# Kernel tuning notes

Hardware: AMD Instinct MI355X
Metric: run time of the kernel (lower is better)

## Reference

```python
import jax, jax.numpy as jnp
import numpy as np

T, B, D, H, N = 2048, 8, 1024, 16, 32


def setup_inputs() -> dict:
    key = jax.random.key(0)
    ks = jax.random.split(key, 6)
    s = 1.0 / np.sqrt(D)  # xavier-ish scale
    return {
        "x": jax.random.normal(ks[0], (T, B, D), jnp.float32),
        "S0": jnp.zeros((B, H, N, N), jnp.float32),
        "W_in": jax.random.normal(ks[1], (D, D), jnp.float32) * s,
        "W_k": jax.random.normal(ks[2], (H * N, D), jnp.float32) * s,
        "W_v": jax.random.normal(ks[3], (H * N, D), jnp.float32) * s,
        "W_q": jax.random.normal(ks[4], (H * N, D), jnp.float32) * s,
        "W_beta": jax.random.normal(ks[5], (H * N, D), jnp.float32) * s,
        "b_beta": jnp.full((H, N), 2.0, jnp.float32),  # init_beta_bias=2.0
    }


def reference(x, S0, W_in, W_k, W_v, W_q, W_beta, b_beta):
    # x: [T,B,D] -> in_proj (expansion=1.0 so d_inner == D)
    Tn, Bn, Dn = x.shape
    Hh, Nn = b_beta.shape
    xp = jnp.einsum('tbd,ed->tbe', x, W_in)  # [T,B,D]
    # projections to [T,B,H,N]
    k = jnp.einsum('tbd,fd->tbf', xp, W_k).reshape(Tn, Bn, Hh, Nn)
    v = jnp.einsum('tbd,fd->tbf', xp, W_v).reshape(Tn, Bn, Hh, Nn)
    q = jnp.einsum('tbd,fd->tbf', xp, W_q).reshape(Tn, Bn, Hh, Nn)
    beta = jax.nn.sigmoid(
        jnp.einsum('tbd,fd->tbf', xp, W_beta).reshape(Tn, Bn, Hh, Nn) + b_beta)

    def step(S, inputs):
        # S: [B,H,N,N]; each input: [B,H,N]
        k_t, v_t, q_t, beta_t = inputs
        k_norm = k_t / (jnp.linalg.norm(k_t, axis=-1, keepdims=True) + 1e-6)
        retrieved = jnp.einsum('bhij,bhj->bhi', S, k_norm)
        delta = v_t - retrieved
        outer = delta[..., :, None] * k_norm[..., None, :]  # [B,H,N,N]
        S_new = jnp.tanh(beta_t[..., None] * S + outer)
        Sq = jnp.einsum('bhij,bhj->bhi', S_new, q_t)
        out_t = Sq * (Sq * jax.nn.sigmoid(Sq))  # Sq * silu(Sq)
        return S_new, out_t

    S_final, outs = jax.lax.scan(step, S0, (k, v, q, beta))
    output = outs.reshape(Tn, Bn, Hh * Nn)  # [T,B,H*N]
    return output, S_final
```

## Files before the change

kernel.cpp:

```cpp
#include <hip/hip_runtime.h>
#include <hip/hip_bf16.h>
#include <stdint.h>

#define TT 2048
#define BB 8
#define DD 1024
#define FF 2048
#define HN 512
#define KB_CNT 32
#define ROWB 128
#define MSTRIDE 4096
#define BROWB 64
#define BSTRIDE 2048
#define PF 8

typedef float f32x4 __attribute__((ext_vector_type(4)));
typedef float f32x2 __attribute__((ext_vector_type(2)));
typedef _Float16 h8_t __attribute__((ext_vector_type(8)));

#define CC   2.88539008f
#define SQC  1.69864360f

__device__ __forceinline__ float fexp2(float x){ return __builtin_amdgcn_exp2f(x); }
__device__ __forceinline__ float frcp(float x){ return __builtin_amdgcn_rcpf(x); }
__device__ __forceinline__ float fsqrt_(float x){ return __builtin_amdgcn_sqrtf(x); }
__device__ __forceinline__ float fast_sigmoid(float x){
    return frcp(1.0f + fexp2(-1.44269504f * x));
}

template<int CTRL>
__device__ __forceinline__ float dppadd(float v){
    int x = __builtin_amdgcn_update_dpp(0, __float_as_int(v), CTRL, 0xf, 0xf, true);
    return v + __int_as_float(x);
}
__device__ __forceinline__ float reduce16(float v){
    v = dppadd<0xB1>(v);
    v = dppadd<0x4E>(v);
    v = dppadd<0x141>(v);
    v = dppadd<0x140>(v);
    return v;
}

__device__ __forceinline__ void split8(const float* f, int4& hi, int4& lo){
    union { _Float16 h[8]; int4 i; } a, c;
    #pragma unroll
    for (int u = 0; u < 8; ++u) {
        _Float16 h = (_Float16)f[u];
        a.h[u] = h;
        c.h[u] = (_Float16)(f[u] - (float)h);
    }
    hi = a.i; lo = c.i;
}
__device__ __forceinline__ int4 cvt8(const float* f){
    union { _Float16 h[8]; int4 i; } a;
    #pragma unroll
    for (int u = 0; u < 8; ++u) a.h[u] = (_Float16)f[u];
    return a.i;
}

__global__ __launch_bounds__(256)
void gemm_f32c(const float* __restrict__ s0, const float* __restrict__ s1,
               const float* __restrict__ s2, const float* __restrict__ s3,
               const float* __restrict__ B, float* __restrict__ C)
{
    __shared__ __align__(16) float As[16][68];
    __shared__ __align__(16) float Bs[16][72];
    const int tid = threadIdx.x;
    const int tx = tid & 15, ty = tid >> 4;
    const int n0 = blockIdx.x * 64, m0 = blockIdx.y * 64;
    float acc[4][4] = {};

    const int arow = tid >> 2, ac4 = (tid & 3) << 2;
    const int f = m0 + arow;
    const float* asrc = ((f < 512) ? s0 : (f < 1024) ? s1 : (f < 1536) ? s2 : s3)
                        + (size_t)(f & 511) * DD + ac4;
    const int bk = tid >> 4, bc = tid & 15;

    for (int k0 = 0; k0 < DD; k0 += 16) {
        float4 av = *(const float4*)(asrc + k0);
        As[ac4+0][arow] = av.x; As[ac4+1][arow] = av.y;
        As[ac4+2][arow] = av.z; As[ac4+3][arow] = av.w;
        float4 bv = *(const float4*)&B[(size_t)(k0 + bk) * DD + n0 + bc * 4];
        int p = bc + (bc >> 3);
        *(float4*)&Bs[bk][p << 2] = bv;
        __syncthreads();
        #pragma unroll
        for (int kk = 0; kk < 16; ++kk) {
            float a[4], b[4];
            *(float4*)&a[0] = *(const float4*)&As[kk][ty * 4];
            int p2 = tx + (tx >> 3);
            *(float4*)&b[0] = *(const float4*)&Bs[kk][p2 << 2];
            #pragma unroll
            for (int i = 0; i < 4; ++i)
                #pragma unroll
                for (int j = 0; j < 4; ++j)
                    acc[i][j] = __builtin_fmaf(a[i], b[j], acc[i][j]);
        }
        __syncthreads();
    }
    #pragma unroll
    for (int ii = 0; ii < 4; ++ii) {
        float4 v;
        v.x = acc[ii][0]; v.y = acc[ii][1]; v.z = acc[ii][2]; v.w = acc[ii][3];
        *(float4*)&C[(size_t)(m0 + ty * 4 + ii) * DD + n0 + tx * 4] = v;
    }
}

__global__ __launch_bounds__(256)
void wconv(const float* __restrict__ W, char* __restrict__ out)
{
    int gid = blockIdx.x * 256 + threadIdx.x;
    int n  = gid >> 6;
    int kh = gid & 63;
    const float* src = W + (size_t)n * DD + kh * 16;
    float f[16];
    *(float4*)&f[0]  = *(const float4*)(src + 0);
    *(float4*)&f[4]  = *(const float4*)(src + 4);
    *(float4*)&f[8]  = *(const float4*)(src + 8);
    *(float4*)&f[12] = *(const float4*)(src + 12);
    int4 hi0, hi1, lo0, lo1;
    split8(&f[0], hi0, lo0);
    split8(&f[8], hi1, lo1);
    int kb = kh >> 1, c0 = (kh & 1) * 2, rs = n & 7;
    char* dst = out + (size_t)n * MSTRIDE + kb * ROWB;
    *(int4*)(dst + (((c0+0) ^ rs) * 16)) = hi0;
    *(int4*)(dst + (((c0+1) ^ rs) * 16)) = hi1;
    *(int4*)(dst + (((c0+4) ^ rs) * 16)) = lo0;
    *(int4*)(dst + (((c0+5) ^ rs) * 16)) = lo1;
}

__global__ __launch_bounds__(256)
void wconv2(const float* __restrict__ W, char* __restrict__ out)
{
    int gid = blockIdx.x * 256 + threadIdx.x;
    int n  = gid >> 6;
    int kh = gid & 63;
    const float* src = W + (size_t)n * DD + kh * 16;
    float f[16];
    *(float4*)&f[0]  = *(const float4*)(src + 0);
    *(float4*)&f[4]  = *(const float4*)(src + 4);
    *(float4*)&f[8]  = *(const float4*)(src + 8);
    *(float4*)&f[12] = *(const float4*)(src + 12);
    int4 h0 = cvt8(&f[0]);
    int4 h1 = cvt8(&f[8]);
    int kb = kh >> 1, c0 = (kh & 1) * 2, rs = n & 3;
    char* dst = out + (size_t)n * BSTRIDE + kb * BROWB;
    *(int4*)(dst + (((c0+0) ^ rs) * 16)) = h0;
    *(int4*)(dst + (((c0+1) ^ rs) * 16)) = h1;
}

#define EPI_STORE(Cb, rbase, reg, hh, idx, blk, v, bb) { \
    char* rowp = (char*)(Cb) + (size_t)((rbase) + (reg)) * 8192 + (hh) * 512; \
    int sub_ = ((blk) == 0) ? 0 : ((blk) == 2) ? 1 : ((blk) == 1) ? 2 : 3; \
    float v_ = (v); \
    if ((blk) == 1) v_ = SQC * v_; \
    else if ((blk) == 3) v_ = CC * fast_sigmoid(v_ + (bb)); \
    *(float*)(rowp + sub_ * 128 + (idx) * 4) = v_; \
}

__global__ __launch_bounds__(512, 1)
void gemm_mfma8(const char* __restrict__ Axp, const char* __restrict__ Wsp,
                float* __restrict__ C, const float* __restrict__ bias)
{
    extern __shared__ char ldsb[];
    const int tid  = threadIdx.x;
    const int wave = tid >> 6, lane = tid & 63;
    const int wm = wave >> 2, wn = wave & 3;
    const int nt = blockIdx.x & 7, mt = blockIdx.x >> 3;
    const int m0 = mt * 256, n0 = nt * 256;

    f32x4 acc[8][4] = {};

    const char* aT = Axp + (size_t)(m0 + wave * 32 + (lane >> 3)) * MSTRIDE + (lane & 7) * 16;
    const char* bT = Wsp + (size_t)(n0 + wave * 32 + (lane >> 2)) * BSTRIDE + (lane & 3) * 16;
    const int ldstA = wave * 32 * 128;
    const int ldstB = wave * 32 * 64;

    const int fl = lane & 15, fh = lane >> 4;
    const int shiA = (fh ^ (fl & 7)) * 16;
    const int sloA = ((fh + 4) ^ (fl & 7)) * 16;
    const int shiB = (fh ^ (fl & 3)) * 16;

    {
        char* L = ldsb;
        #pragma unroll
        for (int g = 0; g < 4; ++g)
            __builtin_amdgcn_global_load_lds(
                (const __attribute__((address_space(1))) uint32_t*)(aT + (size_t)g * 8 * MSTRIDE),
                (__attribute__((address_space(3))) uint32_t*)(L + ldstA + g * 1024),
                16, 0, 0);
        #pragma unroll
        for (int g = 0; g < 2; ++g)
            __builtin_amdgcn_global_load_lds(
                (const __attribute__((address_space(1))) uint32_t*)(bT + (size_t)g * 16 * BSTRIDE),
                (__attribute__((address_space(3))) uint32_t*)(L + 32768 + ldstB + g * 1024),
                16, 0, 0);
    }

    union u8 { int4 i; h8_t h; };
    u8 Ah[4], Al[4], Bf[4];

    for (int t = 0; t < KB_CNT; ++t) {
        char* Lc = ldsb + (t & 1) * 49152;
        char* Ln = ldsb + ((t + 1) & 1) * 49152;
        const bool stg = (t + 1 < KB_CNT);
        const char* aN = aT + ROWB;
        const char* bN = bT + BROWB;

        asm volatile("s_waitcnt vmcnt(0)" ::: "memory");
        __builtin_amdgcn_s_barrier();
        asm volatile("" ::: "memory");

        if (stg) {
            #pragma unroll
            for (int g = 0; g < 4; ++g)
                __builtin_amdgcn_global_load_lds(
                    (const __attribute__((address_space(1))) uint32_t*)(aN + (size_t)g * 8 * MSTRIDE),
                    (__attribute__((address_space(3))) uint32_t*)(Ln + ldstA + g * 1024),
                    16, 0, 0);
            #pragma unroll
            for (int g = 0; g < 2; ++g)
                __builtin_amdgcn_global_load_lds(
                    (const __attribute__((address_space(1))) uint32_t*)(bN + (size_t)g * 16 * BSTRIDE),
                    (__attribute__((address_space(3))) uint32_t*)(Ln + 32768 + ldstB + g * 1024),
                    16, 0, 0);
        }

        #pragma unroll
        for (int f = 0; f < 4; ++f) {
            const char* base = Lc + 32768 + (wn * 64 + f * 16 + fl) * 64;
            Bf[f].i = *(const int4*)(base + shiB);
        }

        #pragma unroll
        for (int f = 0; f < 4; ++f) {
            const char* base = Lc + (wm * 128 + f * 16 + fl) * 128;
            Ah[f].i = *(const int4*)(base + shiA);
            Al[f].i = *(const int4*)(base + sloA);
        }
        __builtin_amdgcn_s_setprio(1);
        #pragma unroll
        for (int i = 0; i < 4; ++i)
            #pragma unroll
            for (int j = 0; j < 4; ++j)
                acc[i][j] = __builtin_amdgcn_mfma_f32_16x16x32_f16(Ah[i].h, Bf[j].h, acc[i][j], 0, 0, 0);
        #pragma unroll
        for (int i = 0; i < 4; ++i)
            #pragma unroll
            for (int j = 0; j < 4; ++j)
                acc[i][j] = __builtin_amdgcn_mfma_f32_16x16x32_f16(Al[i].h, Bf[j].h, acc[i][j], 0, 0, 0);
        __builtin_amdgcn_s_setprio(0);

        #pragma unroll
        for (int f = 0; f < 4; ++f) {
            const char* base = Lc + (wm * 128 + (f + 4) * 16 + fl) * 128;
            Ah[f].i = *(const int4*)(base + shiA);
            Al[f].i = *(const int4*)(base + sloA);
        }
        __builtin_amdgcn_s_setprio(1);
        #pragma unroll
        for (int i = 0; i < 4; ++i)
            #pragma unroll
            for (int j = 0; j < 4; ++j)
                acc[i + 4][j] = __builtin_amdgcn_mfma_f32_16x16x32_f16(Ah[i].h, Bf[j].h, acc[i + 4][j], 0, 0, 0);
        #pragma unroll
        for (int i = 0; i < 4; ++i)
            #pragma unroll
            for (int j = 0; j < 4; ++j)
                acc[i + 4][j] = __builtin_amdgcn_mfma_f32_16x16x32_f16(Al[i].h, Bf[j].h, acc[i + 4][j], 0, 0, 0);
        __builtin_amdgcn_s_setprio(0);

        aT += ROWB; bT += BROWB;
    }

    const int blk = nt >> 1;
    if (blk == 0) {
        #pragma unroll
        for (int fm = 0; fm < 8; ++fm)
            #pragma unroll
            for (int hg = 0; hg < 2; ++hg)
                #pragma unroll
                for (int reg = 0; reg < 4; ++reg) {
                    float a = acc[fm][hg*2][reg], c = acc[fm][hg*2+1][reg];
                    float p = __builtin_fmaf(a, a, c * c);
                    p = reduce16(p);
                    float rn = SQC * frcp(fsqrt_(p) + 1e-6f);
                    acc[fm][hg*2][reg]   = a * rn;
                    acc[fm][hg*2+1][reg] = c * rn;
                }
    }

    #pragma unroll
    for (int fm = 0; fm < 8; ++fm) {
        int rbase = m0 + wm * 128 + fm * 16 + fh * 4;
        #pragma unroll
        for (int fn = 0; fn < 4; ++fn) {
            int col = n0 + wn * 64 + fn * 16 + fl;
            int hh  = (col >> 5) & 15;
            int idx = col & 31;
            float bb = (blk == 3) ? bias[col - 3 * HN] : 0.0f;
            #pragma unroll
            for (int reg = 0; reg < 4; ++reg) {
                float v = acc[fm][fn][reg];
                EPI_STORE(C, rbase, reg, hh, idx, blk, v, bb);
            }
        }
    }
}

__global__ __launch_bounds__(256)
void gemm_mfma(const float* __restrict__ A, const char* __restrict__ Wsp,
               float* __restrict__ C, const float* __restrict__ bias)
{
    __shared__ char lds[24576];
    char* Asb = lds;
    char* Bsb = lds + 16384;

    const int tid  = threadIdx.x;
    const int wave = tid >> 6, lane = tid & 63;
    const int wm = wave >> 1, wn = wave & 1;
    const int nt = blockIdx.x & 15, mt = blockIdx.x >> 4;
    const int m0 = mt * 128, n0 = nt * 128;

    f32x4 acc[4][4] = {};

    const int ar = tid >> 1, akh = tid & 1, ars = ar & 7, ac0 = akh * 2;
    const float* asrc = A + (size_t)(m0 + ar) * DD + akh * 16;
    char* awr = Asb + ar * ROWB;

    const char* bsrc_base = Wsp + (size_t)n0 * BSTRIDE;

    const int fl = lane & 15, fh = lane >> 4;
    const int shiA = (fh ^ (fl & 7)) * 16;
    const int sloA = ((fh + 4) ^ (fl & 7)) * 16;
    const int shiB = (fh ^ (fl & 3)) * 16;

    for (int ks = 0; ks < KB_CNT; ++ks) {
        #pragma unroll
        for (int gg = 0; gg < 2; ++gg) {
            int g = wave * 2 + gg;
            const char* src = bsrc_base + (size_t)(g * 16 + (lane >> 2)) * BSTRIDE
                              + ks * BROWB + (lane & 3) * 16;
            __builtin_amdgcn_global_load_lds(
                (const __attribute__((address_space(1))) uint32_t*)src,
                (__attribute__((address_space(3))) uint32_t*)(Bsb + g * 1024),
                16, 0, 0);
        }
        {
            const float* ap = asrc + ks * 32;
            float f[16];
            *(float4*)&f[0]  = *(const float4*)(ap + 0);
            *(float4*)&f[4]  = *(const float4*)(ap + 4);
            *(float4*)&f[8]  = *(const float4*)(ap + 8);
            *(float4*)&f[12] = *(const float4*)(ap + 12);
            int4 hi0, hi1, lo0, lo1;
            split8(&f[0], hi0, lo0);
            split8(&f[8], hi1, lo1);
            *(int4*)(awr + (((ac0+0) ^ ars) * 16)) = hi0;
            *(int4*)(awr + (((ac0+1) ^ ars) * 16)) = hi1;
            *(int4*)(awr + (((ac0+4) ^ ars) * 16)) = lo0;
            *(int4*)(awr + (((ac0+5) ^ ars) * 16)) = lo1;
        }
        __syncthreads();

        union { int4 i; h8_t h; } ah[4], al[4], bf[4];
        #pragma unroll
        for (int fm = 0; fm < 4; ++fm) {
            const char* base = Asb + (wm * 64 + fm * 16 + fl) * ROWB;
            ah[fm].i = *(const int4*)(base + shiA);
            al[fm].i = *(const int4*)(base + sloA);
        }
        #pragma unroll
        for (int fn = 0; fn < 4; ++fn) {
            const char* base = Bsb + (wn * 64 + fn * 16 + fl) * BROWB;
            bf[fn].i = *(const int4*)(base + shiB);
        }
        #pragma unroll
        for (int fm = 0; fm < 4; ++fm)
            #pragma unroll
            for (int fn = 0; fn < 4; ++fn) {
                acc[fm][fn] = __builtin_amdgcn_mfma_f32_16x16x32_f16(ah[fm].h, bf[fn].h, acc[fm][fn], 0, 0, 0);
                acc[fm][fn] = __builtin_amdgcn_mfma_f32_16x16x32_f16(al[fm].h, bf[fn].h, acc[fm][fn], 0, 0, 0);
            }
        __syncthreads();
    }

    const int blk = nt >> 2;
    if (blk == 0) {
        #pragma unroll
        for (int fm = 0; fm < 4; ++fm)
            #pragma unroll
            for (int hg = 0; hg < 2; ++hg)
                #pragma unroll
                for (int reg = 0; reg < 4; ++reg) {
                    float a = acc[fm][hg*2][reg], c = acc[fm][hg*2+1][reg];
                    float p = __builtin_fmaf(a, a, c * c);
                    p = reduce16(p);
                    float rn = SQC * frcp(fsqrt_(p) + 1e-6f);
                    acc[fm][hg*2][reg]   = a * rn;
                    acc[fm][hg*2+1][reg] = c * rn;
                }
    }

    #pragma unroll
    for (int fm = 0; fm < 4; ++fm) {
        int rbase = m0 + wm * 64 + fm * 16 + fh * 4;
        #pragma unroll
        for (int fn = 0; fn < 4; ++fn) {
            int col = n0 + wn * 64 + fn * 16 + fl;
            int hh  = (col >> 5) & 15;
            int idx = col & 31;
            float bb = (blk == 3) ? bias[col - 3 * HN] : 0.0f;
            #pragma unroll
            for (int reg = 0; reg < 4; ++reg) {
                float v = acc[fm][fn][reg];
                EPI_STORE(C, rbase, reg, hh, idx, blk, v, bb);
            }
        }
    }
}

__global__ __launch_bounds__(256)
void recur(const float* __restrict__ proj, const float* __restrict__ S0,
           float* __restrict__ out, float* __restrict__ Sfin)
{
    const int tid = threadIdx.x;
    const int bx  = blockIdx.x;
    const int bh  = bx >> 1;
    const int b   = bh >> 4, h = bh & 15;
    const int i   = ((bx & 1) << 4) + (tid >> 4);
    const int jl  = tid & 15;

    f32x2 S;
    {
        const float* s0p = S0 + (size_t)bh * 1024 + i * 32 + 2 * jl;
        S[0] = s0p[0]; S[1] = s0p[1];
    }

    const char* pkq = (const char*)proj + (size_t)b * 8192 + h * 512 + jl * 8;
    const char* pvb = (const char*)proj + (size_t)b * 8192 + h * 512 + 256 + i * 4;
    const size_t rstep = (size_t)BB * 8192;

    f32x2 K2[PF], Q2[PF];
    float V[PF], Bt[PF];

    #pragma unroll
    for (int p = 0; p < PF; ++p) {
        asm volatile("global_load_dwordx2 %0, %1, off"            : "=v"(K2[p]) : "v"(pkq));
        asm volatile("global_load_dwordx2 %0, %1, off offset:128" : "=v"(Q2[p]) : "v"(pkq));
        asm volatile("global_load_dword %0, %1, off"              : "=v"(V[p])  : "v"(pvb));
        asm volatile("global_load_dword %0, %1, off offset:128"   : "=v"(Bt[p]) : "v"(pvb));
        pkq += rstep; pvb += rstep;
    }

    asm volatile("s_waitcnt vmcnt(28)" : "+v"(V[0]), "+v"(Bt[0]));
    float cv = V[0];
    f32x2 bS = Bt[0] * S;

    float* pout = out + (size_t)b * HN + h * 32 + i;

    for (int t0 = 0; t0 < TT; t0 += PF) {
        float osave[PF];
        #pragma unroll
        for (int p = 0; p < PF; ++p) {
            const int pn = (p + 1) & (PF - 1);
            asm volatile("s_waitcnt vmcnt(24)"
                : "+v"(K2[p]), "+v"(Q2[p]), "+v"(V[pn]), "+v"(Bt[pn]));

            f32x2 k2 = K2[p];
            float rr = __builtin_fmaf(S[1], k2[1], S[0] * k2[0]);
            rr = reduce16(rr);
            float d = cv - rr;
            f32x2 a = d * k2 + bS;
            f32x2 e; e[0] = fexp2(a[0]); e[1] = fexp2(a[1]);
            f32x2 e1 = e + 1.0f;
            f32x2 r; r[0] = frcp(e1[0]); r[1] = frcp(e1[1]);
            S = -2.0f * r + 1.0f;

            f32x2 q2 = Q2[p];
            osave[p] = __builtin_fmaf(S[1], q2[1], S[0] * q2[0]);

            cv = V[pn];
            bS = Bt[pn] * S;

            asm volatile("global_load_dwordx2 %0, %1, off"            : "=v"(K2[p]) : "v"(pkq));
            asm volatile("global_load_dwordx2 %0, %1, off offset:128" : "=v"(Q2[p]) : "v"(pkq));
            asm volatile("global_load_dword %0, %1, off"              : "=v"(V[p])  : "v"(pvb));
            asm volatile("global_load_dword %0, %1, off offset:128"   : "=v"(Bt[p]) : "v"(pvb));
            pkq += rstep; pvb += rstep;
        }
        #pragma unroll
        for (int p = 0; p < PF; ++p) osave[p] = reduce16(osave[p]);
        if (jl == 0) {
            #pragma unroll
            for (int p = 0; p < PF; ++p) {
                float sq = osave[p];
                float sg = fast_sigmoid(sq);
                pout[(size_t)p * (BB * HN)] = sq * sq * sg;
            }
        }
        pout += (size_t)PF * (BB * HN);
    }

    {
        float* sf = Sfin + (size_t)bh * 1024 + i * 32 + 2 * jl;
        sf[0] = S[0]; sf[1] = S[1];
    }
}

extern "C" void kernel_launch(void* const* d_in, const int* in_sizes, int n_in,
                              void* d_out, int out_size, void* d_ws, size_t ws_size,
                              hipStream_t stream) {
    const float* x      = (const float*)d_in[0];
    const float* S0     = (const float*)d_in[1];
    const float* W_in   = (const float*)d_in[2];
    const float* W_k    = (const float*)d_in[3];
    const float* W_v    = (const float*)d_in[4];
    const float* W_q    = (const float*)d_in[5];
    const float* W_beta = (const float*)d_in[6];
    const float* b_beta = (const float*)d_in[7];

    float* ws   = (float*)d_ws;
    float* out_ = (float*)d_out;
    float* Sfin = out_ + (size_t)TT * BB * HN;

    const size_t NEED_PRE = (size_t)(33554432 + 16777216 + 2*2097152) * 4;
    const bool pre = (ws_size >= NEED_PRE);

    if (pre) {
        float* proj   = ws;
        char*  xsplit = (char*)(ws + 33554432);
        float* Weff   = ws + 33554432 + 16777216;
        char*  wsplit = (char*)(Weff + 2097152);

        hipError_t aerr = hipFuncSetAttribute(
            reinterpret_cast<const void*>(&gemm_mfma8),
            hipFuncAttributeMaxDynamicSharedMemorySize, 98304);

        gemm_f32c<<<dim3(16, 32), dim3(256), 0, stream>>>(W_k, W_v, W_q, W_beta, W_in, Weff);
        wconv2<<<dim3(512), dim3(256), 0, stream>>>(Weff, wsplit);
        wconv<<<dim3(4096), dim3(256), 0, stream>>>(x, xsplit);
        if (aerr == hipSuccess) {
            gemm_mfma8<<<dim3(512), dim3(512), 98304, stream>>>(xsplit, wsplit, proj, b_beta);
        } else {
            gemm_mfma<<<dim3(2048), dim3(256), 0, stream>>>(x, wsplit, proj, b_beta);
        }
        recur<<<dim3(256), dim3(256), 0, stream>>>(proj, S0, out_, Sfin);
    } else {
        float* proj   = ws;
        float* Weff   = ws + 33554432;
        char*  wsplit = (char*)(Weff + 2097152);

        gemm_f32c<<<dim3(16, 32), dim3(256), 0, stream>>>(W_k, W_v, W_q, W_beta, W_in, Weff);
        wconv2<<<dim3(512), dim3(256), 0, stream>>>(Weff, wsplit);
        gemm_mfma<<<dim3(2048), dim3(256), 0, stream>>>(x, wsplit, proj, b_beta);
        recur<<<dim3(256), dim3(256), 0, stream>>>(proj, S0, out_, Sfin);
    }
}
```

Before: 481.8 us.

## Drop hi/lo fp16 split of x, use single fp16 A operand and remap blocks

The activation matrix x was split into fp16 high and low parts, so each K step ran two MFMA passes per A fragment. It is now converted to plain fp16 with the same wconv2 path used for the weights. That halves the A-side LDS footprint, the global traffic and the MFMA count in the projection GEMM. The block index is also remapped so consecutive blocks spread across M tiles while sharing N tiles, which may change L2 reuse. The cost is lower precision on x, which could breach the tolerance given the recurrent tanh dynamics.

```diff
diff --git a/kernel.cpp b/kernel.cpp
--- a/kernel.cpp
+++ b/kernel.cpp
@@ -104,29 +104,6 @@
         v.x = acc[ii][0]; v.y = acc[ii][1]; v.z = acc[ii][2]; v.w = acc[ii][3];
         *(float4*)&C[(size_t)(m0 + ty * 4 + ii) * DD + n0 + tx * 4] = v;
     }
-}
-
-__global__ __launch_bounds__(256)
-void wconv(const float* __restrict__ W, char* __restrict__ out)
-{
-    int gid = blockIdx.x * 256 + threadIdx.x;
-    int n  = gid >> 6;
-    int kh = gid & 63;
-    const float* src = W + (size_t)n * DD + kh * 16;
-    float f[16];
-    *(float4*)&f[0]  = *(const float4*)(src + 0);
-    *(float4*)&f[4]  = *(const float4*)(src + 4);
-    *(float4*)&f[8]  = *(const float4*)(src + 8);
-    *(float4*)&f[12] = *(const float4*)(src + 12);
-    int4 hi0, hi1, lo0, lo1;
-    split8(&f[0], hi0, lo0);
-    split8(&f[8], hi1, lo1);
-    int kb = kh >> 1, c0 = (kh & 1) * 2, rs = n & 7;
-    char* dst = out + (size_t)n * MSTRIDE + kb * ROWB;
-    *(int4*)(dst + (((c0+0) ^ rs) * 16)) = hi0;
-    *(int4*)(dst + (((c0+1) ^ rs) * 16)) = hi1;
-    *(int4*)(dst + (((c0+4) ^ rs) * 16)) = lo0;
-    *(int4*)(dst + (((c0+5) ^ rs) * 16)) = lo1;
 }
 
 __global__ __launch_bounds__(256)
@@ -166,45 +143,45 @@
     const int tid  = threadIdx.x;
     const int wave = tid >> 6, lane = tid & 63;
     const int wm = wave >> 2, wn = wave & 3;
-    const int nt = blockIdx.x & 7, mt = blockIdx.x >> 3;
+    const int d  = blockIdx.x;
+    const int s  = d >> 3;
+    const int mt = (d & 7) * 8 + (s >> 3);
+    const int nt = s & 7;
     const int m0 = mt * 256, n0 = nt * 256;
 
     f32x4 acc[8][4] = {};
 
-    const char* aT = Axp + (size_t)(m0 + wave * 32 + (lane >> 3)) * MSTRIDE + (lane & 7) * 16;
+    const char* aT = Axp + (size_t)(m0 + wave * 32 + (lane >> 2)) * BSTRIDE + (lane & 3) * 16;
     const char* bT = Wsp + (size_t)(n0 + wave * 32 + (lane >> 2)) * BSTRIDE + (lane & 3) * 16;
-    const int ldstA = wave * 32 * 128;
-    const int ldstB = wave * 32 * 64;
+    const int ldst = wave * 32 * 64;
 
     const int fl = lane & 15, fh = lane >> 4;
-    const int shiA = (fh ^ (fl & 7)) * 16;
-    const int sloA = ((fh + 4) ^ (fl & 7)) * 16;
-    const int shiB = (fh ^ (fl & 3)) * 16;
+    const int sslot = (fh ^ (fl & 3)) * 16;
 
     {
         char* L = ldsb;
         #pragma unroll
-        for (int g = 0; g < 4; ++g)
+        for (int g = 0; g < 2; ++g)
             __builtin_amdgcn_global_load_lds(
-                (const __attribute__((address_space(1))) uint32_t*)(aT + (size_t)g * 8 * MSTRIDE),
-                (__attribute__((address_space(3))) uint32_t*)(L + ldstA + g * 1024),
+                (const __attribute__((address_space(1))) uint32_t*)(aT + (size_t)g * 16 * BSTRIDE),
+                (__attribute__((address_space(3))) uint32_t*)(L + ldst + g * 1024),
                 16, 0, 0);
         #pragma unroll
         for (int g = 0; g < 2; ++g)
             __builtin_amdgcn_global_load_lds(
                 (const __attribute__((address_space(1))) uint32_t*)(bT + (size_t)g * 16 * BSTRIDE),
-                (__attribute__((address_space(3))) uint32_t*)(L + 32768 + ldstB + g * 1024),
+                (__attribute__((address_space(3))) uint32_t*)(L + 16384 + ldst + g * 1024),
                 16, 0, 0);
     }
 
     union u8 { int4 i; h8_t h; };
-    u8 Ah[4], Al[4], Bf[4];
+    u8 Af[8], Bf[4];
 
     for (int t = 0; t < KB_CNT; ++t) {
-        char* Lc = ldsb + (t & 1) * 49152;
-        char* Ln = ldsb + ((t + 1) & 1) * 49152;
+        char* Lc = ldsb + (t & 1) * 32768;
+        char* Ln = ldsb + ((t + 1) & 1) * 32768;
         const bool stg = (t + 1 < KB_CNT);
-        const char* aN = aT + ROWB;
+        const char* aN = aT + BROWB;
         const char* bN = bT + BROWB;
 
         asm volatile("s_waitcnt vmcnt(0)" ::: "memory");
@@ -213,64 +190,39 @@
 
         if (stg) {
             #pragma unroll
-            for (int g = 0; g < 4; ++g)
+            for (int g = 0; g < 2; ++g)
                 __builtin_amdgcn_global_load_lds(
-                    (const __attribute__((address_space(1))) uint32_t*)(aN + (size_t)g * 8 * MSTRIDE),
-                    (__attribute__((address_space(3))) uint32_t*)(Ln + ldstA + g * 1024),
+                    (const __attribute__((address_space(1))) uint32_t*)(aN + (size_t)g * 16 * BSTRIDE),
+                    (__attribute__((address_space(3))) uint32_t*)(Ln + ldst + g * 1024),
                     16, 0, 0);
             #pragma unroll
             for (int g = 0; g < 2; ++g)
                 __builtin_amdgcn_global_load_lds(
                     (const __attribute__((address_space(1))) uint32_t*)(bN + (size_t)g * 16 * BSTRIDE),
-                    (__attribute__((address_space(3))) uint32_t*)(Ln + 32768 + ldstB + g * 1024),
+                    (__attribute__((address_space(3))) uint32_t*)(Ln + 16384 + ldst + g * 1024),
                     16, 0, 0);
         }
 
         #pragma unroll
+        for (int f = 0; f < 8; ++f) {
+            const char* base = Lc + (wm * 128 + f * 16 + fl) * 64;
+            Af[f].i = *(const int4*)(base + sslot);
+        }
+        #pragma unroll
         for (int f = 0; f < 4; ++f) {
-            const char* base = Lc + 32768 + (wn * 64 + f * 16 + fl) * 64;
-            Bf[f].i = *(const int4*)(base + shiB);
-        }
-
-        #pragma unroll
-        for (int f = 0; f < 4; ++f) {
-            const char* base = Lc + (wm * 128 + f * 16 + fl) * 128;
-            Ah[f].i = *(const int4*)(base + shiA);
-            Al[f].i = *(const int4*)(base + sloA);
-        }
+            const char* base = Lc + 16384 + (wn * 64 + f * 16 + fl) * 64;
+            Bf[f].i = *(const int4*)(base + sslot);
+        }
+
         __builtin_amdgcn_s_setprio(1);
         #pragma unroll
-        for (int i = 0; i < 4; ++i)
+        for (int i = 0; i < 8; ++i)
             #pragma unroll
             for (int j = 0; j < 4; ++j)
-                acc[i][j] = __builtin_amdgcn_mfma_f32_16x16x32_f16(Ah[i].h, Bf[j].h, acc[i][j], 0, 0, 0);
-        #pragma unroll
-        for (int i = 0; i < 4; ++i)
-            #pragma unroll
-            for (int j = 0; j < 4; ++j)
-                acc[i][j] = __builtin_amdgcn_mfma_f32_16x16x32_f16(Al[i].h, Bf[j].h, acc[i][j], 0, 0, 0);
+                acc[i][j] = __builtin_amdgcn_mfma_f32_16x16x32_f16(Af[i].h, Bf[j].h, acc[i][j], 0, 0, 0);
         __builtin_amdgcn_s_setprio(0);
 
-        #pragma unroll
-        for (int f = 0; f < 4; ++f) {
-            const char* base = Lc + (wm * 128 + (f + 4) * 16 + fl) * 128;
-            Ah[f].i = *(const int4*)(base + shiA);
-            Al[f].i = *(const int4*)(base + sloA);
-        }
-        __builtin_amdgcn_s_setprio(1);
-        #pragma unroll
-        for (int i = 0; i < 4; ++i)
-            #pragma unroll
-            for (int j = 0; j < 4; ++j)
-                acc[i + 4][j] = __builtin_amdgcn_mfma_f32_16x16x32_f16(Ah[i].h, Bf[j].h, acc[i + 4][j], 0, 0, 0);
-        #pragma unroll
-        for (int i = 0; i < 4; ++i)
-            #pragma unroll
-            for (int j = 0; j < 4; ++j)
-                acc[i + 4][j] = __builtin_amdgcn_mfma_f32_16x16x32_f16(Al[i].h, Bf[j].h, acc[i + 4][j], 0, 0, 0);
-        __builtin_amdgcn_s_setprio(0);
-
-        aT += ROWB; bT += BROWB;
+        aT += BROWB; bT += BROWB;
     }
 
     const int blk = nt >> 1;
@@ -535,13 +487,13 @@
 
         hipError_t aerr = hipFuncSetAttribute(
             reinterpret_cast<const void*>(&gemm_mfma8),
-            hipFuncAttributeMaxDynamicSharedMemorySize, 98304);
+            hipFuncAttributeMaxDynamicSharedMemorySize, 65536);
 
         gemm_f32c<<<dim3(16, 32), dim3(256), 0, stream>>>(W_k, W_v, W_q, W_beta, W_in, Weff);
         wconv2<<<dim3(512), dim3(256), 0, stream>>>(Weff, wsplit);
-        wconv<<<dim3(4096), dim3(256), 0, stream>>>(x, xsplit);
+        wconv2<<<dim3(4096), dim3(256), 0, stream>>>(x, xsplit);
         if (aerr == hipSuccess) {
-            gemm_mfma8<<<dim3(512), dim3(512), 98304, stream>>>(xsplit, wsplit, proj, b_beta);
+            gemm_mfma8<<<dim3(512), dim3(512), 65536, stream>>>(xsplit, wsplit, proj, b_beta);
         } else {
             gemm_mfma<<<dim3(2048), dim3(256), 0, stream>>>(x, wsplit, proj, b_beta);
         }
```

New measurement: 430.3 us. 1.12x faster.
